# Optimization experiments

Hardware: AMD Instinct MI355X
Metric: run time of the kernel (lower is better)

## Reference

```python
import jax, jax.numpy as jnp
import numpy as np

B, T, DIM, H, DH = 4, 2048, 1024, 16, 64
NEG = -1.0e9


def setup_inputs() -> dict:
    key = jax.random.key(0)
    ks = jax.random.split(key, 12)
    inner = H * DH
    s_in = 1.0 / np.sqrt(DIM)
    s_out = 1.0 / np.sqrt(inner)
    q = jax.random.normal(ks[0], (B, T, DIM), jnp.float32)
    k = jax.random.normal(ks[1], (B, T, DIM), jnp.float32)
    v = jax.random.normal(ks[2], (B, T, DIM), jnp.float32)
    # nn.Linear weights stored as [out, in]; we keep [in, out] for x @ W
    W_q = jax.random.uniform(ks[3], (DIM, inner), jnp.float32, -s_in, s_in)
    b_q = jax.random.uniform(ks[4], (inner,), jnp.float32, -s_in, s_in)
    W_k = jax.random.uniform(ks[5], (DIM, inner), jnp.float32, -s_in, s_in)
    b_k = jax.random.uniform(ks[6], (inner,), jnp.float32, -s_in, s_in)
    W_v = jax.random.uniform(ks[7], (DIM, inner), jnp.float32, -s_in, s_in)
    b_v = jax.random.uniform(ks[8], (inner,), jnp.float32, -s_in, s_in)
    W_o = jax.random.uniform(ks[9], (inner, DIM), jnp.float32, -s_out, s_out)
    b_o = jax.random.uniform(ks[10], (DIM,), jnp.float32, -s_out, s_out)
    # causal mask: True = masked (strict upper triangle), broadcastable [1,1,T,T]
    causal_mask = jnp.triu(jnp.ones((T, T), bool), k=1)[None, None]
    # context mask: True = keep; random padding pattern with col 0 always valid
    context_mask = jax.random.bernoulli(ks[11], 0.9, (B, T)).at[:, 0].set(True)
    return {"q": q, "k": k, "v": v,
            "W_q": W_q, "b_q": b_q, "W_k": W_k, "b_k": b_k,
            "W_v": W_v, "b_v": b_v, "W_o": W_o, "b_o": b_o,
            "causal_mask": causal_mask, "context_mask": context_mask}


def reference(q, k, v, W_q, b_q, W_k, b_k, W_v, b_v, W_o, b_o,
              causal_mask, context_mask):
    scale = DH ** -0.5
    split = lambda x: x.reshape(x.shape[0], x.shape[1], H, DH).transpose(0, 2, 1, 3)
    qh = split(q @ W_q + b_q)  # [b,h,t,d]
    kh = split(k @ W_k + b_k)
    vh = split(v @ W_v + b_v)
    scores = jnp.einsum('bhid,bhjd->bhij', qh * scale, kh)
    scores = jnp.where(context_mask[:, None, None, :], scores, NEG)
    scores = jnp.where(causal_mask, NEG, scores)
    probs = jax.nn.softmax(scores, axis=-1)
    out = jnp.einsum('bhij,bhjd->bhid', probs, vh)
    out = out.transpose(0, 2, 1, 3).reshape(B, T, H * DH)
    return out @ W_o + b_o
```

## Files before the change

kernel.cpp:

```cpp
#include <hip/hip_runtime.h>
#include <hip/hip_bf16.h>
#include <cstdint>
#include <cstddef>

#define DEV static __device__ __forceinline__

typedef __attribute__((ext_vector_type(8))) short short8;
typedef __attribute__((ext_vector_type(4))) short short4v;
typedef __attribute__((ext_vector_type(4))) float floatx4;

#define BB 4
#define TT 2048
#define DIMM 1024
#define HH 16
#define DHH 64
#define MM (BB*TT)
#define QBLK 256
#define NQT (TT/QBLK)
#define M0F 12.0f

DEV unsigned short f2bu(float f) {
    unsigned int u = __float_as_uint(f);
    unsigned int r = (u + 0x7fffu + ((u >> 16) & 1u)) >> 16;
    return (unsigned short)r;
}

DEV unsigned long long pack4(float a, float b, float c, float d) {
    return (unsigned long long)f2bu(a) | ((unsigned long long)f2bu(b) << 16) |
           ((unsigned long long)f2bu(c) << 32) | ((unsigned long long)f2bu(d) << 48);
}

DEV unsigned int pk2(float lo, float hi) {
    __hip_bfloat162 h = __float22bfloat162_rn(make_float2(lo, hi));
    unsigned int r;
    __builtin_memcpy(&r, &h, 4);
    return r;
}

DEV unsigned long long pk4(float a, float b, float c, float d) {
    return (unsigned long long)pk2(a, b) | ((unsigned long long)pk2(c, d) << 32);
}

DEV void gload16(const void* g, void* l) {
    __builtin_amdgcn_global_load_lds(
        (const __attribute__((address_space(1))) unsigned int*)g,
        (__attribute__((address_space(3))) unsigned int*)l, 16, 0, 0);
}

#define MFMA16(a, b, c) __builtin_amdgcn_mfma_f32_16x16x32_bf16((a), (b), (c), 0, 0, 0)

#if defined(__has_builtin)
#if __has_builtin(__builtin_amdgcn_mfma_f32_16x16x16bf16_1k)
#define HAVE_MFMA_K16 1
#endif
#endif

DEV floatx4 mfma_k16(short4v a, short4v b, floatx4 c) {
#ifdef HAVE_MFMA_K16
    return __builtin_amdgcn_mfma_f32_16x16x16bf16_1k(a, b, c, 0, 0, 0);
#else
    asm volatile("v_mfma_f32_16x16x16_bf16 %0, %1, %2, %0" : "+v"(c) : "v"(a), "v"(b));
    return c;
#endif
}

__global__ __launch_bounds__(256) void ctx_bias(const unsigned char* __restrict__ raw,
                                                float* __restrict__ out) {
    __shared__ int nz1, nz23;
    if (threadIdx.x == 0) { nz1 = 0; nz23 = 0; }
    __syncthreads();
    int a1 = 0, a23 = 0;
    for (int i = threadIdx.x; i < BB * TT; i += 256) {
        unsigned char vb = raw[i];
        int m = i & 3;
        if (vb) { if (m == 1) a1 = 1; else if (m >= 2) a23 = 1; }
    }
    if (a1) atomicOr(&nz1, 1);
    if (a23) atomicOr(&nz23, 1);
    __syncthreads();
    const int mode = nz1 ? 2 : (nz23 ? 1 : 0);
    for (int i = threadIdx.x; i < BB * TT; i += 256) {
        bool keep;
        if (mode == 2)      keep = raw[i] != 0;
        else if (mode == 0) keep = raw[(size_t)4 * i] != 0;
        else                keep = (raw[(size_t)4 * i + 2] | raw[(size_t)4 * i + 3]) != 0;
        out[i] = keep ? -M0F : -3.0e38f;
    }
}

__global__ __launch_bounds__(256) void wtrans(const float* __restrict__ W0, const float* __restrict__ W1,
                                              const float* __restrict__ W2, const float* __restrict__ W3,
                                              unsigned short* __restrict__ out) {
    const float* W = blockIdx.y == 0 ? W0 : blockIdx.y == 1 ? W1 : blockIdx.y == 2 ? W2 : W3;
    unsigned short* O = out + (size_t)blockIdx.y * DIMM * DIMM;
    const int tx = blockIdx.x & 15, ty = blockIdx.x >> 4;
    __shared__ float s[64][65];
    const int tid = threadIdx.x;
#pragma unroll
    for (int j = 0; j < 4; ++j) {
        int c = tid + 256 * j;
        int r = c >> 4, c4 = c & 15;
        float4 vv = *reinterpret_cast<const float4*>(&W[(size_t)(ty * 64 + r) * DIMM + tx * 64 + c4 * 4]);
        s[r][c4 * 4 + 0] = vv.x; s[r][c4 * 4 + 1] = vv.y;
        s[r][c4 * 4 + 2] = vv.z; s[r][c4 * 4 + 3] = vv.w;
    }
    __syncthreads();
#pragma unroll
    for (int j = 0; j < 4; ++j) {
        int c = tid + 256 * j;
        int n = c >> 4, k4 = c & 15;
        unsigned long long pk = pack4(s[k4 * 4 + 0][n], s[k4 * 4 + 1][n], s[k4 * 4 + 2][n], s[k4 * 4 + 3][n]);
        *reinterpret_cast<unsigned long long*>(&O[(size_t)(tx * 64 + n) * DIMM + ty * 64 + k4 * 4]) = pk;
    }
}

__global__ __launch_bounds__(256) void cvt_bf16(const float* __restrict__ in,
                                                unsigned short* __restrict__ out) {
    const size_t i = ((size_t)blockIdx.x * 256 + threadIdx.x) * 8;
    float4 a = *reinterpret_cast<const float4*>(&in[i]);
    float4 b = *reinterpret_cast<const float4*>(&in[i + 4]);
    unsigned long long lo = pk4(a.x, a.y, a.z, a.w);
    unsigned long long hi = pk4(b.x, b.y, b.z, b.w);
    ulonglong2 v; v.x = lo; v.y = hi;
    *reinterpret_cast<ulonglong2*>(&out[i]) = v;
}

template <int OMODE>
__global__ __launch_bounds__(256) void gemm_bf16(const unsigned short* __restrict__ Ab,
                                                 const unsigned short* __restrict__ Bt,
                                                 const float* __restrict__ bias,
                                                 void* __restrict__ Cp, float scale) {
    __shared__ unsigned short As[2][128 * 64];
    __shared__ unsigned short Bs[2][128 * 64];
    const int tid = threadIdx.x, lane = tid & 63, g = lane >> 4, lq = lane & 15;
    const int wid = tid >> 6;
    const int mbase = blockIdx.x * 128, nbase = blockIdx.y * 128;
    const int wm = (wid >> 1) * 64, wn = (wid & 1) * 64;
    floatx4 acc[4][4];
#pragma unroll
    for (int i = 0; i < 4; ++i)
#pragma unroll
        for (int j = 0; j < 4; ++j) acc[i][j] = (floatx4){0.f, 0.f, 0.f, 0.f};

#define STAGE(buf, k0)                                                              \
    {                                                                               \
        _Pragma("unroll")                                                           \
        for (int j = 0; j < 4; ++j) {                                               \
            const int c = j * 256 + tid;                                            \
            const int row = c >> 3, ci = c & 7;                                     \
            const int sc = ci ^ (row & 7);                                          \
            gload16(&Ab[(size_t)(mbase + row) * DIMM + (k0) + sc * 8], &As[buf][c * 8]); \
            gload16(&Bt[(size_t)(nbase + row) * DIMM + (k0) + sc * 8], &Bs[buf][c * 8]); \
        }                                                                           \
    }

    STAGE(0, 0);
    asm volatile("s_waitcnt vmcnt(0)");
    __syncthreads();
    int cur = 0;
    for (int k0 = 0; k0 < DIMM; k0 += 64) {
        if (k0 + 64 < DIMM) STAGE(cur ^ 1, k0 + 64);
#pragma unroll
        for (int kk = 0; kk < 2; ++kk) {
            short8 af[4], bf[4];
#pragma unroll
            for (int i = 0; i < 4; ++i) {
                const int ra = wm + i * 16 + lq;
                af[i] = *reinterpret_cast<const short8*>(&As[cur][ra * 64 + ((kk * 4 + g) ^ (ra & 7)) * 8]);
                const int rb = wn + i * 16 + lq;
                bf[i] = *reinterpret_cast<const short8*>(&Bs[cur][rb * 64 + ((kk * 4 + g) ^ (rb & 7)) * 8]);
            }
#pragma unroll
            for (int i = 0; i < 4; ++i)
#pragma unroll
                for (int j2 = 0; j2 < 4; ++j2)
                    acc[i][j2] = MFMA16(af[i], bf[j2], acc[i][j2]);
        }
        __syncthreads();
        cur ^= 1;
    }
#undef STAGE

#pragma unroll
    for (int i = 0; i < 4; ++i) {
#pragma unroll
        for (int j = 0; j < 4; ++j) {
            const int col = nbase + wn + j * 16 + lq;
            const float bvv = bias[col];
            const int row0 = mbase + wm + i * 16 + g * 4;
            if (OMODE == 2) {
                float* C = (float*)Cp;
#pragma unroll
                for (int r = 0; r < 4; ++r)
                    C[(size_t)(row0 + r) * DIMM + col] = acc[i][j][r] + bvv;
            } else if (OMODE == 0) {
                unsigned short* C = (unsigned short*)Cp;
#pragma unroll
                for (int r = 0; r < 4; ++r)
                    C[(size_t)(row0 + r) * DIMM + col] = f2bu((acc[i][j][r] + bvv) * scale);
            } else {
                unsigned short* C = (unsigned short*)Cp;
                const int b = row0 >> 11, t0 = row0 & (TT - 1);
                const int h = col >> 6, d = col & 63;
                unsigned long long pk = pk4(acc[i][j][0] + bvv, acc[i][j][1] + bvv,
                                            acc[i][j][2] + bvv, acc[i][j][3] + bvv);
                *reinterpret_cast<unsigned long long*>(
                    &C[((size_t)(b * HH + h) * DHH + d) * TT + t0]) = pk;
            }
        }
    }
}

__global__ __launch_bounds__(512) void attn256(const unsigned short* __restrict__ Q,
                                               const unsigned short* __restrict__ Km,
                                               const unsigned short* __restrict__ Vt,
                                               const float* __restrict__ ctxb,
                                               unsigned short* __restrict__ O) {
    const int bh = blockIdx.x & 63, qtIdx = blockIdx.x >> 6;
    const int h = bh & 15, b = bh >> 4;
    const int low = qtIdx & 3, hi = qtIdx >> 2;
    const int off = ((low & 1) << 1) | (low >> 1);
    const int qt = hi == 0 ? 7 - off : off;
    const int tid = threadIdx.x, lane = tid & 63, g = lane >> 4, lq = lane & 15, wid = tid >> 6;

    __shared__ unsigned short Ks[2][64 * 64];
    __shared__ unsigned short Vs[2][64 * 64];
    __shared__ float sbias[TT];

    const unsigned short* Vbase = Vt + (size_t)(b * HH + h) * DHH * TT;
    const int srow = tid >> 3, sdc = tid & 7;
    const int soff = (srow * 128 + sdc * 16) ^ ((srow & 7) << 4);

    const int qbase = qt * QBLK;
    const size_t rowQ = (size_t)(b * TT + qbase);
    const int nkv = 4 * qt + 4;

    *reinterpret_cast<float4*>(&sbias[tid * 4]) =
        *reinterpret_cast<const float4*>(&ctxb[b * TT + tid * 4]);
    {
        float4 k0v = *reinterpret_cast<const float4*>(&Km[(size_t)(b * TT + srow) * DIMM + h * DHH + sdc * 8]);
        float4 v0v = *reinterpret_cast<const float4*>(&Vbase[(size_t)srow * TT + sdc * 8]);
        *reinterpret_cast<float4*>((char*)Ks[0] + soff) = k0v;
        *reinterpret_cast<float4*>((char*)Vs[0] + soff) = v0v;
    }
    const int qra = wid * 32 + lq;
    short8 qa0 = *reinterpret_cast<const short8*>(&Q[(rowQ + qra) * DIMM + h * DHH + g * 8]);
    short8 qa1 = *reinterpret_cast<const short8*>(&Q[(rowQ + qra) * DIMM + h * DHH + 32 + g * 8]);
    short8 qb0 = *reinterpret_cast<const short8*>(&Q[(rowQ + qra + 16) * DIMM + h * DHH + g * 8]);
    short8 qb1 = *reinterpret_cast<const short8*>(&Q[(rowQ + qra + 16) * DIMM + h * DHH + 32 + g * 8]);
    __syncthreads();

    floatx4 oa[4], ob[4];
#pragma unroll
    for (int f = 0; f < 4; ++f) { oa[f] = (floatx4){0.f,0.f,0.f,0.f}; ob[f] = (floatx4){0.f,0.f,0.f,0.f}; }
    float l_a = 0.f, l_b = 0.f;
    const int qwave = qbase + wid * 32;
    const int qg_a = qwave + lq, qg_b = qg_a + 16;

    for (int kt = 0; kt < nkv; ++kt) {
        const int cur = kt & 1;
        const int kvb = kt * 64;
        const bool pf = (kt + 1 < nkv);
        float4 kreg, vreg;
        if (pf) {
            const int kvn = kvb + 64;
            kreg = *reinterpret_cast<const float4*>(&Km[(size_t)(b * TT + kvn + srow) * DIMM + h * DHH + sdc * 8]);
            vreg = *reinterpret_cast<const float4*>(&Vbase[(size_t)srow * TT + kvn + sdc * 8]);
        }
        if (kvb <= qwave + 31) {
            const bool nCa = (kvb + 63 > qwave);
            const bool nCb = (kvb + 63 > qwave + 16);
            short4v wa[4], wb[4];
            float rs_a = 0.f, rs_b = 0.f;
            __builtin_amdgcn_s_setprio(1);
#pragma unroll
            for (int f = 0; f < 4; ++f) {
                const int r = f * 16 + lq;
                const int sw = (r & 7) << 4;
                short8 kf0 = *reinterpret_cast<const short8*>((char*)Ks[cur] + ((r * 128 + g * 16) ^ sw));
                short8 kf1 = *reinterpret_cast<const short8*>((char*)Ks[cur] + ((r * 128 + 64 + g * 16) ^ sw));
                const float4 bias = *reinterpret_cast<const float4*>(&sbias[kvb + f * 16 + g * 4]);
                floatx4 binit = (floatx4){bias.x, bias.y, bias.z, bias.w};
                floatx4 ta = MFMA16(kf1, qa1, MFMA16(kf0, qa0, binit));
                floatx4 tb = MFMA16(kf1, qb1, MFMA16(kf0, qb0, binit));
                float pa[4], pb[4];
#pragma unroll
                for (int r2 = 0; r2 < 4; ++r2) {
                    const int kv = kvb + f * 16 + g * 4 + r2;
                    float sa = ta[r2], sb = tb[r2];
                    if (nCa && kv > qg_a) sa = -3.0e38f;
                    if (nCb && kv > qg_b) sb = -3.0e38f;
                    pa[r2] = exp2f(sa);
                    pb[r2] = exp2f(sb);
                    rs_a += pa[r2];
                    rs_b += pb[r2];
                }
                unsigned long long wav = pk4(pa[0], pa[1], pa[2], pa[3]);
                unsigned long long wbv = pk4(pb[0], pb[1], pb[2], pb[3]);
                __builtin_memcpy(&wa[f], &wav, 8);
                __builtin_memcpy(&wb[f], &wbv, 8);
            }
            __builtin_amdgcn_s_setprio(0);
            rs_a += __shfl_xor(rs_a, 16, 64);
            rs_a += __shfl_xor(rs_a, 32, 64);
            rs_b += __shfl_xor(rs_b, 16, 64);
            rs_b += __shfl_xor(rs_b, 32, 64);
            l_a += rs_a;
            l_b += rs_b;
            __builtin_amdgcn_s_setprio(1);
#pragma unroll
            for (int f = 0; f < 4; ++f) {
                const int r = f * 16 + lq;
                const int sw = (r & 7) << 4;
                const int rb = r * 128;
#pragma unroll
                for (int j = 0; j < 4; ++j) {
                    short4v av = *reinterpret_cast<const short4v*>(
                        (char*)Vs[cur] + ((rb + j * 32 + g * 8) ^ sw));
                    oa[f] = mfma_k16(av, wa[j], oa[f]);
                    ob[f] = mfma_k16(av, wb[j], ob[f]);
                }
            }
            __builtin_amdgcn_s_setprio(0);
#ifndef HAVE_MFMA_K16
            asm volatile("s_nop 7\ns_nop 7");
#endif
        }
        if (pf) {
            *reinterpret_cast<float4*>((char*)Ks[cur ^ 1] + soff) = kreg;
            *reinterpret_cast<float4*>((char*)Vs[cur ^ 1] + soff) = vreg;
        }
        __syncthreads();
    }

    const float ia = 1.f / l_a, ib = 1.f / l_b;
#pragma unroll
    for (int f = 0; f < 4; ++f) {
        unsigned long long pka = pk4(oa[f][0] * ia, oa[f][1] * ia, oa[f][2] * ia, oa[f][3] * ia);
        unsigned long long pkb = pk4(ob[f][0] * ib, ob[f][1] * ib, ob[f][2] * ib, ob[f][3] * ib);
        *reinterpret_cast<unsigned long long*>(
            &O[(rowQ + qra) * DIMM + h * DHH + f * 16 + g * 4]) = pka;
        *reinterpret_cast<unsigned long long*>(
            &O[(rowQ + qra + 16) * DIMM + h * DHH + f * 16 + g * 4]) = pkb;
    }
}

extern "C" void kernel_launch(void* const* d_in, const int* in_sizes, int n_in,
                              void* d_out, int out_size, void* d_ws, size_t ws_size,
                              hipStream_t stream) {
    const float* q  = (const float*)d_in[0];
    const float* k  = (const float*)d_in[1];
    const float* v  = (const float*)d_in[2];
    const float* Wq = (const float*)d_in[3];
    const float* bq = (const float*)d_in[4];
    const float* Wk = (const float*)d_in[5];
    const float* bk = (const float*)d_in[6];
    const float* Wv = (const float*)d_in[7];
    const float* bv = (const float*)d_in[8];
    const float* Wo = (const float*)d_in[9];
    const float* bo = (const float*)d_in[10];
    const unsigned char* cmask = (const unsigned char*)d_in[12];

    unsigned short* Qp  = (unsigned short*)d_ws;
    unsigned short* Kp  = Qp + (size_t)MM * DIMM;
    unsigned short* Vtp = Kp + (size_t)MM * DIMM;
    unsigned short* AO  = Vtp + (size_t)MM * DIMM;
    unsigned short* Wt  = AO + (size_t)MM * DIMM;
    float* ctxb = (float*)(Wt + (size_t)4 * DIMM * DIMM);

    ctx_bias<<<dim3(1), dim3(256), 0, stream>>>(cmask, ctxb);
    wtrans<<<dim3(256, 4), dim3(256), 0, stream>>>(Wq, Wk, Wv, Wo, Wt);

    const float scale_q = 0.125f * 1.4426950408889634f;

    cvt_bf16<<<dim3(4096), dim3(256), 0, stream>>>(q, AO);
    gemm_bf16<0><<<dim3(64, 8), dim3(256), 0, stream>>>(AO, Wt,                           bq, Qp,  scale_q);
    cvt_bf16<<<dim3(4096), dim3(256), 0, stream>>>(k, AO);
    gemm_bf16<0><<<dim3(64, 8), dim3(256), 0, stream>>>(AO, Wt + (size_t)DIMM * DIMM,     bk, Kp,  1.f);
    cvt_bf16<<<dim3(4096), dim3(256), 0, stream>>>(v, AO);
    gemm_bf16<1><<<dim3(64, 8), dim3(256), 0, stream>>>(AO, Wt + (size_t)2 * DIMM * DIMM, bv, Vtp, 1.f);

    attn256<<<dim3(BB * HH * NQT), dim3(512), 0, stream>>>(Qp, Kp, Vtp, ctxb, AO);

    gemm_bf16<2><<<dim3(64, 8), dim3(256), 0, stream>>>(AO, Wt + (size_t)3 * DIMM * DIMM, bo, d_out, 1.f);
}
```

Baseline: 247.8 us.

## Halve attention query tile to 128 rows with 256-thread blocks and 4 blocks/CU

Shrinks the attention query block from 256 to 128 rows, so each block now runs 4 waves of 256 threads instead of 8, and the grid has twice as many blocks. Each thread now loads two K/V chunks per stage to fill the 64-row tiles. The causal tile ordering is changed to interleave heavy and light query tiles across 16 tiles, and launch bounds request 4 blocks per CU. The aim is finer-grained load balance across the causal triangle and better occupancy. The cost is that K/V tiles are reloaded by twice as many blocks, raising global traffic.

```diff
diff --git a/kernel.cpp b/kernel.cpp
--- a/kernel.cpp
+++ b/kernel.cpp
@@ -15,7 +15,7 @@
 #define HH 16
 #define DHH 64
 #define MM (BB*TT)
-#define QBLK 256
+#define QBLK 128
 #define NQT (TT/QBLK)
 #define M0F 12.0f
 
@@ -211,16 +211,15 @@
     }
 }
 
-__global__ __launch_bounds__(512) void attn256(const unsigned short* __restrict__ Q,
-                                               const unsigned short* __restrict__ Km,
-                                               const unsigned short* __restrict__ Vt,
-                                               const float* __restrict__ ctxb,
-                                               unsigned short* __restrict__ O) {
+__global__ __launch_bounds__(256, 4) void attn_v4(const unsigned short* __restrict__ Q,
+                                                  const unsigned short* __restrict__ Km,
+                                                  const unsigned short* __restrict__ Vt,
+                                                  const float* __restrict__ ctxb,
+                                                  unsigned short* __restrict__ O) {
     const int bh = blockIdx.x & 63, qtIdx = blockIdx.x >> 6;
     const int h = bh & 15, b = bh >> 4;
-    const int low = qtIdx & 3, hi = qtIdx >> 2;
-    const int off = ((low & 1) << 1) | (low >> 1);
-    const int qt = hi == 0 ? 7 - off : off;
+    const int jj = qtIdx >> 2, ii = qtIdx & 3;
+    const int qt = jj == 0 ? 15 - ii : jj == 1 ? 8 + ii : jj == 2 ? 7 - ii : ii;
     const int tid = threadIdx.x, lane = tid & 63, g = lane >> 4, lq = lane & 15, wid = tid >> 6;
 
     __shared__ unsigned short Ks[2][64 * 64];
@@ -228,20 +227,29 @@
     __shared__ float sbias[TT];
 
     const unsigned short* Vbase = Vt + (size_t)(b * HH + h) * DHH * TT;
-    const int srow = tid >> 3, sdc = tid & 7;
-    const int soff = (srow * 128 + sdc * 16) ^ ((srow & 7) << 4);
+
+    int srow[2], sdc[2], soff[2];
+#pragma unroll
+    for (int j = 0; j < 2; ++j) {
+        const int c = j * 256 + tid;
+        srow[j] = c >> 3; sdc[j] = c & 7;
+        soff[j] = (srow[j] * 128 + sdc[j] * 16) ^ ((srow[j] & 7) << 4);
+    }
 
     const int qbase = qt * QBLK;
     const size_t rowQ = (size_t)(b * TT + qbase);
-    const int nkv = 4 * qt + 4;
-
-    *reinterpret_cast<float4*>(&sbias[tid * 4]) =
-        *reinterpret_cast<const float4*>(&ctxb[b * TT + tid * 4]);
-    {
-        float4 k0v = *reinterpret_cast<const float4*>(&Km[(size_t)(b * TT + srow) * DIMM + h * DHH + sdc * 8]);
-        float4 v0v = *reinterpret_cast<const float4*>(&Vbase[(size_t)srow * TT + sdc * 8]);
-        *reinterpret_cast<float4*>((char*)Ks[0] + soff) = k0v;
-        *reinterpret_cast<float4*>((char*)Vs[0] + soff) = v0v;
+    const int nkv = 2 * qt + 2;
+
+    *reinterpret_cast<float4*>(&sbias[tid * 8]) =
+        *reinterpret_cast<const float4*>(&ctxb[b * TT + tid * 8]);
+    *reinterpret_cast<float4*>(&sbias[tid * 8 + 4]) =
+        *reinterpret_cast<const float4*>(&ctxb[b * TT + tid * 8 + 4]);
+#pragma unroll
+    for (int j = 0; j < 2; ++j) {
+        *reinterpret_cast<float4*>((char*)Ks[0] + soff[j]) =
+            *reinterpret_cast<const float4*>(&Km[(size_t)(b * TT + srow[j]) * DIMM + h * DHH + sdc[j] * 8]);
+        *reinterpret_cast<float4*>((char*)Vs[0] + soff[j]) =
+            *reinterpret_cast<const float4*>(&Vbase[(size_t)srow[j] * TT + sdc[j] * 8]);
     }
     const int qra = wid * 32 + lq;
     short8 qa0 = *reinterpret_cast<const short8*>(&Q[(rowQ + qra) * DIMM + h * DHH + g * 8]);
@@ -261,11 +269,14 @@
         const int cur = kt & 1;
         const int kvb = kt * 64;
         const bool pf = (kt + 1 < nkv);
-        float4 kreg, vreg;
+        float4 kreg[2], vreg[2];
         if (pf) {
             const int kvn = kvb + 64;
-            kreg = *reinterpret_cast<const float4*>(&Km[(size_t)(b * TT + kvn + srow) * DIMM + h * DHH + sdc * 8]);
-            vreg = *reinterpret_cast<const float4*>(&Vbase[(size_t)srow * TT + kvn + sdc * 8]);
+#pragma unroll
+            for (int j = 0; j < 2; ++j) {
+                kreg[j] = *reinterpret_cast<const float4*>(&Km[(size_t)(b * TT + kvn + srow[j]) * DIMM + h * DHH + sdc[j] * 8]);
+                vreg[j] = *reinterpret_cast<const float4*>(&Vbase[(size_t)srow[j] * TT + kvn + sdc[j] * 8]);
+            }
         }
         if (kvb <= qwave + 31) {
             const bool nCa = (kvb + 63 > qwave);
@@ -327,8 +338,11 @@
 #endif
         }
         if (pf) {
-            *reinterpret_cast<float4*>((char*)Ks[cur ^ 1] + soff) = kreg;
-            *reinterpret_cast<float4*>((char*)Vs[cur ^ 1] + soff) = vreg;
+#pragma unroll
+            for (int j = 0; j < 2; ++j) {
+                *reinterpret_cast<float4*>((char*)Ks[cur ^ 1] + soff[j]) = kreg[j];
+                *reinterpret_cast<float4*>((char*)Vs[cur ^ 1] + soff[j]) = vreg[j];
+            }
         }
         __syncthreads();
     }
@@ -380,7 +394,7 @@
     cvt_bf16<<<dim3(4096), dim3(256), 0, stream>>>(v, AO);
     gemm_bf16<1><<<dim3(64, 8), dim3(256), 0, stream>>>(AO, Wt + (size_t)2 * DIMM * DIMM, bv, Vtp, 1.f);
 
-    attn256<<<dim3(BB * HH * NQT), dim3(512), 0, stream>>>(Qp, Kp, Vtp, ctxb, AO);
+    attn_v4<<<dim3(BB * HH * NQT), dim3(256), 0, stream>>>(Qp, Kp, Vtp, ctxb, AO);
 
     gemm_bf16<2><<<dim3(64, 8), dim3(256), 0, stream>>>(AO, Wt + (size_t)3 * DIMM * DIMM, bo, d_out, 1.f);
 }
```

After: 305.1 us. +23.1%, slower.
